# Performance work log

Measured on AMD Instinct MI355X. Metric: run time of the kernel, lower is better.

## Reference

```python
import jax, jax.numpy as jnp
import numpy as np

B, P, Q, N, D = 64, 12, 12, 1024, 64
DOW, TOD = 7, 288  # day-of-week / time-of-day one-hot depths (GMAN STEmbedding)


def setup_inputs() -> dict:
    key = jax.random.key(0)
    ks = iter(jax.random.split(key, 40))
    def g(shape, scale=0.05):
        return jax.random.normal(next(ks), shape, jnp.float32) * scale
    inp = {
        "X": jax.random.normal(next(ks), (B, P, N), jnp.float32),
        "ZC": jax.random.normal(next(ks), (B, P, 400), jnp.float32),
        "ZF": jax.random.normal(next(ks), (B, P, 1600), jnp.float32),
        "SE": g((N, D)),
        # STEmbedding FCs
        "W_se1": g((D, D)), "b_se1": jnp.zeros((D,), jnp.float32),
        "W_se2": g((D, D)), "b_se2": jnp.zeros((D,), jnp.float32),
        "W_te1": g((DOW + TOD, D)), "b_te1": jnp.zeros((D,), jnp.float32),
        "W_te2": g((D, D)), "b_te2": jnp.zeros((D,), jnp.float32),
        # FC_X_in
        "W_in1": g((1, D)), "b_in1": jnp.zeros((D,), jnp.float32),
        "W_in2": g((D, D)), "b_in2": jnp.zeros((D,), jnp.float32),
        # DCGRU layer 1 (gconv over [x||state, support@(x||state)] -> 4D input)
        "Wg1": g((4 * D, 2 * D)), "bg1": jnp.ones((2 * D,), jnp.float32),
        "Wc1": g((4 * D, D)), "bc1": jnp.zeros((D,), jnp.float32),
        # DCGRU layer 2
        "Wg2": g((4 * D, 2 * D)), "bg2": jnp.ones((2 * D,), jnp.float32),
        "Wc2": g((4 * D, D)), "bc2": jnp.zeros((D,), jnp.float32),
        # FC_X_out
        "W_o1": g((D, D)), "b_o1": jnp.zeros((D,), jnp.float32),
        "W_o2": g((D, Q)), "b_o2": jnp.zeros((Q,), jnp.float32),
        "TE": jax.random.randint(next(ks), (B, P + Q, 2), 0, 7, jnp.int32),
    }
    return inp


def _dcgru_scan(x_seq, support, Wg, bg, Wc, bc):
    """x_seq: [B,P,N,D] -> (sequence [B,P,N,D], last state [B,N,D])."""
    def gconv(x, s, W, b):
        z = jnp.concatenate([x, s], -1)                      # [B,N,2D]
        z1 = jnp.einsum('nm,bmd->bnd', support, z)           # diffusion step K=1
        return jnp.concatenate([z, z1], -1) @ W + b

    def step(state, x_t):
        ru = jax.nn.sigmoid(gconv(x_t, state, Wg, bg))       # [B,N,2D]
        r, u = jnp.split(ru, 2, axis=-1)
        c = jnp.tanh(gconv(x_t, r * state, Wc, bc))
        new = u * state + (1.0 - u) * c
        return new, new

    state0 = jnp.zeros(x_seq.shape[:1] + x_seq.shape[2:], x_seq.dtype)
    last, seq = jax.lax.scan(step, state0, jnp.swapaxes(x_seq, 0, 1))
    return jnp.swapaxes(seq, 0, 1), last


def reference(X, ZC, ZF, SE, W_se1, b_se1, W_se2, b_se2, W_te1, b_te1,
              W_te2, b_te2, W_in1, b_in1, W_in2, b_in2,
              Wg1, bg1, Wc1, bc1, Wg2, bg2, Wc2, bc2,
              W_o1, b_o1, W_o2, b_o2, TE):
    # adjacency is identity in this module; random_walk(I).T == I
    adj = jnp.eye(N, dtype=jnp.float32)
    support = (adj / jnp.sum(adj, axis=1, keepdims=True)).T

    # STEmbedding: spatial + temporal embedding
    se = jax.nn.relu(SE @ W_se1 + b_se1) @ W_se2 + b_se2                 # [N,D]
    te_oh = jnp.concatenate([
        jax.nn.one_hot(TE[..., 0], DOW, dtype=jnp.float32),
        jax.nn.one_hot(TE[..., 1], TOD, dtype=jnp.float32)], -1)        # [B,P+Q,295]
    te = jax.nn.relu(te_oh @ W_te1 + b_te1) @ W_te2 + b_te2              # [B,P+Q,D]
    STEX = (se[None, None] + te[:, :, None, :])[:, :P]                   # [B,P,N,D]

    # FC_X_in on expanded X, add STE
    Xe = X[..., None]                                                    # [B,P,N,1]
    Xe = jax.nn.relu(Xe @ W_in1 + b_in1) @ W_in2 + b_in2                 # [B,P,N,D]
    Xe = Xe + STEX

    seq1, _ = _dcgru_scan(Xe, support, Wg1, bg1, Wc1, bc1)               # [B,P,N,D]
    _, h = _dcgru_scan(seq1, support, Wg2, bg2, Wc2, bc2)                # [B,N,D]

    Y = jax.nn.relu(h @ W_o1 + b_o1) @ W_o2 + b_o2                       # [B,N,Q]
    return jnp.transpose(Y, (0, 2, 1))                                   # [B,Q,N]
```

## Files before the change

kernel.cpp:

```cpp
#include <hip/hip_runtime.h>


#define NB 1024

typedef float f32x4 __attribute__((ext_vector_type(4)));
typedef __bf16 bf16x8 __attribute__((ext_vector_type(8)));
typedef int i32x4 __attribute__((ext_vector_type(4)));
typedef unsigned int u32;
typedef unsigned short u16;

#define MFMA(a, b, c) __builtin_amdgcn_mfma_f32_16x16x32_bf16(a, b, c, 0, 0, 0)

__device__ __forceinline__ float fexp(float x) {
    return __builtin_amdgcn_exp2f(x * 1.44269504088896341f);
}
__device__ __forceinline__ float fsigmoid(float x) {
    return __builtin_amdgcn_rcpf(1.0f + fexp(-x));
}
__device__ __forceinline__ float ftanh(float x) {
    return 1.0f - 2.0f * __builtin_amdgcn_rcpf(1.0f + fexp(2.0f * x));
}

__device__ __forceinline__ u32 packf(float v) {
    u32 u = __builtin_bit_cast(u32, v);
    u32 hb = u & 0xFFFF0000u;
    float lo = v - __builtin_bit_cast(float, hb);
    return hb | (__builtin_bit_cast(u32, lo) >> 16);
}
__device__ __forceinline__ float unpackf(u32 u) {
    return __builtin_bit_cast(float, u & 0xFFFF0000u)
         + __builtin_bit_cast(float, u << 16);
}

__device__ __forceinline__ bf16x8 ldfrag(const u16* p) {
    i32x4 t = *(const i32x4*)p;
    return __builtin_bit_cast(bf16x8, t);
}
__device__ __forceinline__ bf16x8 ldfragL(const u32* p) {
    i32x4 t = *(const i32x4*)p;
    return __builtin_bit_cast(bf16x8, t);
}
__device__ __forceinline__ void split8(f32x4 a0, f32x4 a1, bf16x8& hi, bf16x8& lo) {
    #pragma unroll
    for (int i = 0; i < 4; i++) {
        __bf16 h0 = (__bf16)a0[i]; hi[i] = h0;     lo[i] = (__bf16)(a0[i] - (float)h0);
        __bf16 h1 = (__bf16)a1[i]; hi[4 + i] = h1; lo[4 + i] = (__bf16)(a1[i] - (float)h1);
    }
}

#define SWZ(t) ((((t) & 3) << 3) ^ ((t) & 4) ^ (((t) & 8) << 1))
#define SW(t, k) ((t) * 64 + ((k) ^ SWZ(t)))

__device__ __forceinline__ void lda_packed(const u32* __restrict__ src, int m, int kk,
                                           bf16x8& hi, bf16x8& lo) {
    const int sk = kk ^ SWZ(m);
    i32x4 d0 = *(const i32x4*)(src + m * 64 + sk);
    i32x4 d1 = *(const i32x4*)(src + m * 64 + (sk ^ 4));
    i32x4 h, L;
    h[0] = (int)__builtin_amdgcn_perm((u32)d0[1], (u32)d0[0], 0x07060302u);
    h[1] = (int)__builtin_amdgcn_perm((u32)d0[3], (u32)d0[2], 0x07060302u);
    h[2] = (int)__builtin_amdgcn_perm((u32)d1[1], (u32)d1[0], 0x07060302u);
    h[3] = (int)__builtin_amdgcn_perm((u32)d1[3], (u32)d1[2], 0x07060302u);
    L[0] = (int)__builtin_amdgcn_perm((u32)d0[1], (u32)d0[0], 0x05040100u);
    L[1] = (int)__builtin_amdgcn_perm((u32)d0[3], (u32)d0[2], 0x05040100u);
    L[2] = (int)__builtin_amdgcn_perm((u32)d1[1], (u32)d1[0], 0x05040100u);
    L[3] = (int)__builtin_amdgcn_perm((u32)d1[3], (u32)d1[2], 0x05040100u);
    hi = __builtin_bit_cast(bf16x8, h);
    lo = __builtin_bit_cast(bf16x8, L);
}


__device__ __forceinline__ void wsplit(float v, u16* dhi, u16* dlo) {
    __bf16 h = (__bf16)v;
    __bf16 l = (__bf16)(v - (float)h);
    *dhi = __builtin_bit_cast(u16, h);
    *dlo = __builtin_bit_cast(u16, l);
}

__global__ void prep_gates(const float* __restrict__ Wg1, const float* __restrict__ Wg2,
                           u16* __restrict__ fr) {
    int i = blockIdx.x * 256 + threadIdx.x;
    if (i >= 4096) return;
    int layer = i >> 11, r = i & 2047;
    int w = r >> 9; r &= 511; int nt = r >> 8; r &= 255; int ks = r >> 6; int lane = r & 63;
    const float* Wg = layer ? Wg2 : Wg1;
    int n = lane & 15, q = lane >> 4;
    int col = nt ? (64 + w * 16 + n) : (w * 16 + n);
    u16* dst = fr + layer * 32768 + (((w * 2 + nt) * 4 + ks) * 2) * 512 + lane * 8;
    #pragma unroll
    for (int j = 0; j < 8; j++) {
        int k = ks * 32 + q * 8 + j;
        float v = Wg[k * 128 + col] + Wg[(k + 128) * 128 + col];
        wsplit(v, dst + j, dst + 512 + j);
    }
}

__global__ void prep_cand(const float* __restrict__ Wc1, const float* __restrict__ Wc2,
                          u16* __restrict__ fr) {
    int i = blockIdx.x * 256 + threadIdx.x;
    if (i >= 2048) return;
    int layer = i >> 10, r = i & 1023;
    int w = r >> 8; r &= 255; int ks = r >> 6; int lane = r & 63;
    const float* Wc = layer ? Wc2 : Wc1;
    int n = lane & 15, q = lane >> 4;
    int col = w * 16 + n;
    u16* dst = fr + 65536 + layer * 16384 + ((w * 4 + ks) * 2) * 512 + lane * 8;
    #pragma unroll
    for (int j = 0; j < 8; j++) {
        int k = ks * 32 + q * 8 + j;
        float v = Wc[k * 64 + col] + Wc[(k + 128) * 64 + col];
        wsplit(v, dst + j, dst + 512 + j);
    }
}

__global__ void prep_small(const float* __restrict__ Win2, const float* __restrict__ Wo1,
                           u16* __restrict__ fr) {
    int i = blockIdx.x * 256 + threadIdx.x;
    if (i >= 1024) return;
    int kind = i >> 9, r = i & 511;
    int w = r >> 7; r &= 127; int ks = r >> 6; int lane = r & 63;
    const float* W = kind ? Wo1 : Win2;
    int n = lane & 15, q = lane >> 4;
    int col = w * 16 + n;
    u16* dst = fr + 98304 + kind * 8192 + ((w * 2 + ks) * 2) * 512 + lane * 8;
    #pragma unroll
    for (int j = 0; j < 8; j++) {
        int k = ks * 32 + q * 8 + j;
        float v = W[k * 64 + col];
        wsplit(v, dst + j, dst + 512 + j);
    }
}

__global__ void prep_se(const float* __restrict__ SE, const float* __restrict__ W1,
                        const float* __restrict__ b1, const float* __restrict__ W2,
                        const float* __restrict__ b2, const float* __restrict__ bin2,
                        float* __restrict__ seB) {
    __shared__ float h[64];
    int n = blockIdx.x, d = threadIdx.x;
    float acc = b1[d];
    for (int k = 0; k < 64; k++) acc = fmaf(SE[n * 64 + k], W1[k * 64 + d], acc);
    h[d] = fmaxf(acc, 0.0f);
    __syncthreads();
    float acc2 = b2[d];
    for (int k = 0; k < 64; k++) acc2 = fmaf(h[k], W2[k * 64 + d], acc2);
    int nb = n >> 6, tok = n & 63;
    int mt = tok >> 4, q = (tok >> 2) & 3, r = tok & 3;
    int w = d >> 4, n16 = d & 15;
    seB[(((nb * 4 + w) * 64) + q * 16 + n16) * 16 + mt * 4 + r] = acc2 + bin2[d];
}

__global__ void prep_te(const int* __restrict__ TE, const float* __restrict__ W1,
                        const float* __restrict__ b1, const float* __restrict__ W2,
                        const float* __restrict__ b2, float* __restrict__ teo) {
    __shared__ float h[64];
    int bp = blockIdx.x;
    int b = bp / 12, p = bp - b * 12;
    int d = threadIdx.x;
    int dow = TE[(b * 24 + p) * 2 + 0];
    int tod = TE[(b * 24 + p) * 2 + 1];
    float v = W1[dow * 64 + d] + W1[(7 + tod) * 64 + d] + b1[d];
    h[d] = fmaxf(v, 0.0f);
    __syncthreads();
    float acc = b2[d];
    for (int k = 0; k < 64; k++) acc = fmaf(h[k], W2[k * 64 + d], acc);
    teo[bp * 64 + d] = acc;
}

__device__ __forceinline__ void gru_full(
    const u32* __restrict__ XIN, u32* __restrict__ S, u32* __restrict__ RS,
    const u16* __restrict__ frG, const u16* __restrict__ frC,
    float bgr, float bgu, float bcc, int l, int col) {
    const int n16 = l & 15, q = l >> 4;
    f32x4 accR[4], accU[4], accC[4];
    #pragma unroll
    for (int mt = 0; mt < 4; mt++) {
        accR[mt] = (f32x4)0.0f; accU[mt] = (f32x4)0.0f; accC[mt] = (f32x4)0.0f;
    }
    #pragma unroll
    for (int ks = 0; ks < 2; ks++) {
        bf16x8 gRh = ldfrag(frG + (ks * 2 + 0) * 512 + l * 8);
        bf16x8 gRl = ldfrag(frG + (ks * 2 + 1) * 512 + l * 8);
        bf16x8 gUh = ldfrag(frG + (8 + ks * 2 + 0) * 512 + l * 8);
        bf16x8 gUl = ldfrag(frG + (8 + ks * 2 + 1) * 512 + l * 8);
        bf16x8 bhiC = ldfrag(frC + (ks * 2 + 0) * 512 + l * 8);
        bf16x8 bloC = ldfrag(frC + (ks * 2 + 1) * 512 + l * 8);
        const int kk = ks * 32 + q * 8;
        #pragma unroll
        for (int mt = 0; mt < 4; mt++) {
            bf16x8 ahi, alo;
            lda_packed(XIN, mt * 16 + n16, kk, ahi, alo);
            accR[mt] = MFMA(ahi, gRh, accR[mt]);
            accR[mt] = MFMA(alo, gRh, accR[mt]);
            accR[mt] = MFMA(ahi, gRl, accR[mt]);
            accU[mt] = MFMA(ahi, gUh, accU[mt]);
            accU[mt] = MFMA(alo, gUh, accU[mt]);
            accU[mt] = MFMA(ahi, gUl, accU[mt]);
            accC[mt] = MFMA(ahi, bhiC, accC[mt]);
            accC[mt] = MFMA(alo, bhiC, accC[mt]);
            accC[mt] = MFMA(ahi, bloC, accC[mt]);
        }
    }
    #pragma unroll
    for (int ks = 2; ks < 4; ks++) {
        bf16x8 gRh = ldfrag(frG + (ks * 2 + 0) * 512 + l * 8);
        bf16x8 gRl = ldfrag(frG + (ks * 2 + 1) * 512 + l * 8);
        bf16x8 gUh = ldfrag(frG + (8 + ks * 2 + 0) * 512 + l * 8);
        bf16x8 gUl = ldfrag(frG + (8 + ks * 2 + 1) * 512 + l * 8);
        const int kk = (ks - 2) * 32 + q * 8;
        #pragma unroll
        for (int mt = 0; mt < 4; mt++) {
            bf16x8 ahi, alo;
            lda_packed(S, mt * 16 + n16, kk, ahi, alo);
            accR[mt] = MFMA(ahi, gRh, accR[mt]);
            accR[mt] = MFMA(alo, gRh, accR[mt]);
            accR[mt] = MFMA(ahi, gRl, accR[mt]);
            accU[mt] = MFMA(ahi, gUh, accU[mt]);
            accU[mt] = MFMA(alo, gUh, accU[mt]);
            accU[mt] = MFMA(ahi, gUl, accU[mt]);
        }
    }
    #pragma unroll
    for (int mt = 0; mt < 4; mt++)
        #pragma unroll
        for (int r = 0; r < 4; r++) {
            int tok = mt * 16 + q * 4 + r;
            int a = SW(tok, col);
            RS[a] = packf(fsigmoid(accR[mt][r] + bgr) * unpackf(S[a]));
        }
    __syncthreads();
    #pragma unroll
    for (int ks = 2; ks < 4; ks++) {
        bf16x8 bhi = ldfrag(frC + (ks * 2 + 0) * 512 + l * 8);
        bf16x8 blo = ldfrag(frC + (ks * 2 + 1) * 512 + l * 8);
        const int kk = (ks - 2) * 32 + q * 8;
        #pragma unroll
        for (int mt = 0; mt < 4; mt++) {
            bf16x8 ahi, alo;
            lda_packed(RS, mt * 16 + n16, kk, ahi, alo);
            accC[mt] = MFMA(ahi, bhi, accC[mt]);
            accC[mt] = MFMA(alo, bhi, accC[mt]);
            accC[mt] = MFMA(ahi, blo, accC[mt]);
        }
    }
    #pragma unroll
    for (int mt = 0; mt < 4; mt++)
        #pragma unroll
        for (int r = 0; r < 4; r++) {
            int tok = mt * 16 + q * 4 + r;
            int a = SW(tok, col);
            float u = fsigmoid(accU[mt][r] + bgu);
            float cnd = ftanh(accC[mt][r] + bcc);
            float sold = unpackf(S[a]);
            S[a] = packf(u * sold + (1.0f - u) * cnd);
        }
    __syncthreads();
}

__global__ __launch_bounds__(256, 2) void gman_main(
    const float* __restrict__ X, const float* __restrict__ ws,
    const float* __restrict__ Win1, const float* __restrict__ bin1,
    const float* __restrict__ bg1, const float* __restrict__ bc1,
    const float* __restrict__ bg2, const float* __restrict__ bc2,
    const float* __restrict__ bo1, const float* __restrict__ Wo2,
    const float* __restrict__ bo2, float* __restrict__ out) {
    __shared__ u32 XE[4096], S1[4096], S2[4096], RS[4096];
    __shared__ u32 FRX[4096];

    const int tid = threadIdx.x;
    const int l = tid & 63;
    const int w = tid >> 6;
    const int uw = __builtin_amdgcn_readfirstlane(w);
    const int n16 = l & 15, q = l >> 4;
    const int col = uw * 16 + n16;
    const int b = blockIdx.x >> 4;
    const int nb = blockIdx.x & 15;
    const int n0 = nb << 6;

    const u16* frU = (const u16*)ws;
    const u16* frG1 = frU + uw * 8192;
    const u16* frG2 = frU + 32768 + uw * 8192;
    const u16* frC1 = frU + 65536 + uw * 4096;
    const u16* frC2 = frU + 81920 + uw * 4096;
    const u16* frH  = frU + 106496 + uw * 2048;
    const float* seQ = ws + 57344 + (((nb * 4 + uw) * 64) + l) * 16;
    const float* teo = ws + 122880;

    const u32* frXsrc = (const u32*)ws + 49152;
    #pragma unroll
    for (int i = 0; i < 16; i++) FRX[tid + i * 256] = frXsrc[tid + i * 256];
    const u32* frXL = FRX + uw * 1024;

    #pragma unroll
    for (int i = 0; i < 16; i++) { S1[tid + i * 256] = 0u; S2[tid + i * 256] = 0u; }

    f32x4 se_v[4];
    #pragma unroll
    for (int mt = 0; mt < 4; mt++) se_v[mt] = *(const f32x4*)(seQ + mt * 4);
    const float bg1r = bg1[col], bg1u = bg1[64 + col], bc1c = bc1[col];
    const float bg2r = bg2[col], bg2u = bg2[64 + col], bc2c = bc2[col];

    #pragma unroll 1
    for (int p = 0; p < 12; p++) {
        if (tid < 64) RS[tid] = __builtin_bit_cast(u32, X[(b * 12 + p) * NB + n0 + tid]);
        __syncthreads();
        f32x4 accX[4];
        #pragma unroll
        for (int mt = 0; mt < 4; mt++) accX[mt] = (f32x4)0.0f;
        #pragma unroll
        for (int ks = 0; ks < 2; ks++) {
            const int k0 = ks * 32 + q * 8;
            f32x4 w1a = *(const f32x4*)(Win1 + k0), w1b = *(const f32x4*)(Win1 + k0 + 4);
            f32x4 b1a = *(const f32x4*)(bin1 + k0), b1b = *(const f32x4*)(bin1 + k0 + 4);
            bf16x8 bhi = ldfragL(frXL + (ks * 2 + 0) * 256 + l * 4);
            bf16x8 blo = ldfragL(frXL + (ks * 2 + 1) * 256 + l * 4);
            #pragma unroll
            for (int mt = 0; mt < 4; mt++) {
                const float xm = __builtin_bit_cast(float, RS[mt * 16 + n16]);
                f32x4 h0, h1v;
                #pragma unroll
                for (int i = 0; i < 4; i++) {
                    h0[i]  = fmaxf(fmaf(xm, w1a[i], b1a[i]), 0.0f);
                    h1v[i] = fmaxf(fmaf(xm, w1b[i], b1b[i]), 0.0f);
                }
                bf16x8 ahi, alo; split8(h0, h1v, ahi, alo);
                accX[mt] = MFMA(ahi, bhi, accX[mt]);
                accX[mt] = MFMA(alo, bhi, accX[mt]);
                accX[mt] = MFMA(ahi, blo, accX[mt]);
            }
        }
        const float tev = teo[(b * 12 + p) * 64 + col];
        __syncthreads();
        #pragma unroll
        for (int mt = 0; mt < 4; mt++)
            #pragma unroll
            for (int r = 0; r < 4; r++) {
                int tok = mt * 16 + q * 4 + r;
                XE[SW(tok, col)] = packf(accX[mt][r] + se_v[mt][r] + tev);
            }
        __syncthreads();

        gru_full(XE, S1, RS, frG1, frC1, bg1r, bg1u, bc1c, l, col);
        gru_full(S1, S2, RS, frG2, frC2, bg2r, bg2u, bc2c, l, col);
    }

    f32x4 accH[4];
    #pragma unroll
    for (int mt = 0; mt < 4; mt++) accH[mt] = (f32x4)0.0f;
    #pragma unroll
    for (int ks = 0; ks < 2; ks++) {
        bf16x8 bhi = ldfrag(frH + (ks * 2 + 0) * 512 + l * 8);
        bf16x8 blo = ldfrag(frH + (ks * 2 + 1) * 512 + l * 8);
        const int kk = ks * 32 + q * 8;
        #pragma unroll
        for (int mt = 0; mt < 4; mt++) {
            bf16x8 ahi, alo;
            lda_packed(S2, mt * 16 + n16, kk, ahi, alo);
            accH[mt] = MFMA(ahi, bhi, accH[mt]);
            accH[mt] = MFMA(alo, bhi, accH[mt]);
            accH[mt] = MFMA(ahi, blo, accH[mt]);
        }
    }
    const float bo1c = bo1[col];
    #pragma unroll
    for (int mt = 0; mt < 4; mt++)
        #pragma unroll
        for (int r = 0; r < 4; r++) {
            int tok = mt * 16 + q * 4 + r;
            XE[SW(tok, col)] = packf(fmaxf(accH[mt][r] + bo1c, 0.0f));
        }
    __syncthreads();
    const int swzt = SWZ(l);
    float y0 = bo2[3 * uw + 0], y1 = bo2[3 * uw + 1], y2 = bo2[3 * uw + 2];
    #pragma unroll
    for (int c = 0; c < 16; c++) {
        i32x4 d = *(const i32x4*)(XE + l * 64 + c * 4);
        const int j0 = (c * 4) ^ swzt;
        #pragma unroll
        for (int e = 0; e < 4; e++) {
            float hj = unpackf((u32)d[e]);
            int j = j0 + e;
            y0 = fmaf(hj, Wo2[j * 12 + 3 * uw + 0], y0);
            y1 = fmaf(hj, Wo2[j * 12 + 3 * uw + 1], y1);
            y2 = fmaf(hj, Wo2[j * 12 + 3 * uw + 2], y2);
        }
    }
    out[(b * 12 + 3 * uw + 0) * NB + n0 + l] = y0;
    out[(b * 12 + 3 * uw + 1) * NB + n0 + l] = y1;
    out[(b * 12 + 3 * uw + 2) * NB + n0 + l] = y2;
}

extern "C" void kernel_launch(void* const* d_in, const int* in_sizes, int n_in,
                              void* d_out, int out_size, void* d_ws, size_t ws_size,
                              hipStream_t stream) {
    const float* X    = (const float*)d_in[0];
    const float* SE   = (const float*)d_in[3];
    const float* Wse1 = (const float*)d_in[4];
    const float* bse1 = (const float*)d_in[5];
    const float* Wse2 = (const float*)d_in[6];
    const float* bse2 = (const float*)d_in[7];
    const float* Wte1 = (const float*)d_in[8];
    const float* bte1 = (const float*)d_in[9];
    const float* Wte2 = (const float*)d_in[10];
    const float* bte2 = (const float*)d_in[11];
    const float* Win1 = (const float*)d_in[12];
    const float* bin1 = (const float*)d_in[13];
    const float* Win2 = (const float*)d_in[14];
    const float* bin2 = (const float*)d_in[15];
    const float* Wg1  = (const float*)d_in[16];
    const float* bg1  = (const float*)d_in[17];
    const float* Wc1  = (const float*)d_in[18];
    const float* bc1  = (const float*)d_in[19];
    const float* Wg2  = (const float*)d_in[20];
    const float* bg2  = (const float*)d_in[21];
    const float* Wc2  = (const float*)d_in[22];
    const float* bc2  = (const float*)d_in[23];
    const float* Wo1  = (const float*)d_in[24];
    const float* bo1  = (const float*)d_in[25];
    const float* Wo2  = (const float*)d_in[26];
    const float* bo2  = (const float*)d_in[27];
    const int*   TE   = (const int*)d_in[28];

    float* ws = (float*)d_ws;
    u16* fr = (u16*)ws;
    float* seB = ws + 57344;
    float* teo = ws + 122880;
    float* out = (float*)d_out;

    prep_gates<<<16, 256, 0, stream>>>(Wg1, Wg2, fr);
    prep_cand<<<8, 256, 0, stream>>>(Wc1, Wc2, fr);
    prep_small<<<4, 256, 0, stream>>>(Win2, Wo1, fr);
    prep_se<<<1024, 64, 0, stream>>>(SE, Wse1, bse1, Wse2, bse2, bin2, seB);
    prep_te<<<768, 64, 0, stream>>>(TE, Wte1, bte1, Wte2, bte2, teo);
    gman_main<<<1024, 256, 0, stream>>>(X, ws, Win1, bin1, bg1, bc1, bg2, bc2,
                                        bo1, Wo2, bo2, out);
}
```

Measured before the change: 554.8 us.

## Split each block's 64 tokens across two wave groups using 512 threads

Doubles the block to 512 threads (8 waves). Each group of four waves takes half of the 64 node tokens, which halves the per-wave MFMA M-tiles and accumulator registers in the GRU steps, the input projection and the output head. The goal is more waves per block to hide MFMA and LDS latency in the serial recurrence. In exchange, the same B-fragment weights are loaded by twice as many waves, and the 80KB of shared memory per block may limit how many blocks fit on each CU.

```diff
diff --git a/kernel.cpp b/kernel.cpp
--- a/kernel.cpp
+++ b/kernel.cpp
@@ -169,11 +169,11 @@
 __device__ __forceinline__ void gru_full(
     const u32* __restrict__ XIN, u32* __restrict__ S, u32* __restrict__ RS,
     const u16* __restrict__ frG, const u16* __restrict__ frC,
-    float bgr, float bgu, float bcc, int l, int col) {
+    float bgr, float bgu, float bcc, int l, int col, int mh) {
     const int n16 = l & 15, q = l >> 4;
-    f32x4 accR[4], accU[4], accC[4];
-    #pragma unroll
-    for (int mt = 0; mt < 4; mt++) {
+    f32x4 accR[2], accU[2], accC[2];
+    #pragma unroll
+    for (int mt = 0; mt < 2; mt++) {
         accR[mt] = (f32x4)0.0f; accU[mt] = (f32x4)0.0f; accC[mt] = (f32x4)0.0f;
     }
     #pragma unroll
@@ -186,9 +186,9 @@
         bf16x8 bloC = ldfrag(frC + (ks * 2 + 1) * 512 + l * 8);
         const int kk = ks * 32 + q * 8;
         #pragma unroll
-        for (int mt = 0; mt < 4; mt++) {
+        for (int mt = 0; mt < 2; mt++) {
             bf16x8 ahi, alo;
-            lda_packed(XIN, mt * 16 + n16, kk, ahi, alo);
+            lda_packed(XIN, mh * 32 + mt * 16 + n16, kk, ahi, alo);
             accR[mt] = MFMA(ahi, gRh, accR[mt]);
             accR[mt] = MFMA(alo, gRh, accR[mt]);
             accR[mt] = MFMA(ahi, gRl, accR[mt]);
@@ -208,9 +208,9 @@
         bf16x8 gUl = ldfrag(frG + (8 + ks * 2 + 1) * 512 + l * 8);
         const int kk = (ks - 2) * 32 + q * 8;
         #pragma unroll
-        for (int mt = 0; mt < 4; mt++) {
+        for (int mt = 0; mt < 2; mt++) {
             bf16x8 ahi, alo;
-            lda_packed(S, mt * 16 + n16, kk, ahi, alo);
+            lda_packed(S, mh * 32 + mt * 16 + n16, kk, ahi, alo);
             accR[mt] = MFMA(ahi, gRh, accR[mt]);
             accR[mt] = MFMA(alo, gRh, accR[mt]);
             accR[mt] = MFMA(ahi, gRl, accR[mt]);
@@ -220,10 +220,10 @@
         }
     }
     #pragma unroll
-    for (int mt = 0; mt < 4; mt++)
+    for (int mt = 0; mt < 2; mt++)
         #pragma unroll
         for (int r = 0; r < 4; r++) {
-            int tok = mt * 16 + q * 4 + r;
+            int tok = mh * 32 + mt * 16 + q * 4 + r;
             int a = SW(tok, col);
             RS[a] = packf(fsigmoid(accR[mt][r] + bgr) * unpackf(S[a]));
         }
@@ -234,19 +234,19 @@
         bf16x8 blo = ldfrag(frC + (ks * 2 + 1) * 512 + l * 8);
         const int kk = (ks - 2) * 32 + q * 8;
         #pragma unroll
-        for (int mt = 0; mt < 4; mt++) {
+        for (int mt = 0; mt < 2; mt++) {
             bf16x8 ahi, alo;
-            lda_packed(RS, mt * 16 + n16, kk, ahi, alo);
+            lda_packed(RS, mh * 32 + mt * 16 + n16, kk, ahi, alo);
             accC[mt] = MFMA(ahi, bhi, accC[mt]);
             accC[mt] = MFMA(alo, bhi, accC[mt]);
             accC[mt] = MFMA(ahi, blo, accC[mt]);
         }
     }
     #pragma unroll
-    for (int mt = 0; mt < 4; mt++)
+    for (int mt = 0; mt < 2; mt++)
         #pragma unroll
         for (int r = 0; r < 4; r++) {
-            int tok = mt * 16 + q * 4 + r;
+            int tok = mh * 32 + mt * 16 + q * 4 + r;
             int a = SW(tok, col);
             float u = fsigmoid(accU[mt][r] + bgu);
             float cnd = ftanh(accC[mt][r] + bcc);
@@ -256,7 +256,7 @@
     __syncthreads();
 }
 
-__global__ __launch_bounds__(256, 2) void gman_main(
+__global__ __launch_bounds__(512, 2) void gman_main(
     const float* __restrict__ X, const float* __restrict__ ws,
     const float* __restrict__ Win1, const float* __restrict__ bin1,
     const float* __restrict__ bg1, const float* __restrict__ bc1,
@@ -270,32 +270,34 @@
     const int l = tid & 63;
     const int w = tid >> 6;
     const int uw = __builtin_amdgcn_readfirstlane(w);
+    const int uq = uw & 3;
+    const int mh = uw >> 2;
     const int n16 = l & 15, q = l >> 4;
-    const int col = uw * 16 + n16;
+    const int col = uq * 16 + n16;
     const int b = blockIdx.x >> 4;
     const int nb = blockIdx.x & 15;
     const int n0 = nb << 6;
 
     const u16* frU = (const u16*)ws;
-    const u16* frG1 = frU + uw * 8192;
-    const u16* frG2 = frU + 32768 + uw * 8192;
-    const u16* frC1 = frU + 65536 + uw * 4096;
-    const u16* frC2 = frU + 81920 + uw * 4096;
-    const u16* frH  = frU + 106496 + uw * 2048;
-    const float* seQ = ws + 57344 + (((nb * 4 + uw) * 64) + l) * 16;
+    const u16* frG1 = frU + uq * 8192;
+    const u16* frG2 = frU + 32768 + uq * 8192;
+    const u16* frC1 = frU + 65536 + uq * 4096;
+    const u16* frC2 = frU + 81920 + uq * 4096;
+    const u16* frH  = frU + 106496 + uq * 2048;
+    const float* seQ = ws + 57344 + (((nb * 4 + uq) * 64) + l) * 16;
     const float* teo = ws + 122880;
 
     const u32* frXsrc = (const u32*)ws + 49152;
     #pragma unroll
-    for (int i = 0; i < 16; i++) FRX[tid + i * 256] = frXsrc[tid + i * 256];
-    const u32* frXL = FRX + uw * 1024;
-
-    #pragma unroll
-    for (int i = 0; i < 16; i++) { S1[tid + i * 256] = 0u; S2[tid + i * 256] = 0u; }
-
-    f32x4 se_v[4];
-    #pragma unroll
-    for (int mt = 0; mt < 4; mt++) se_v[mt] = *(const f32x4*)(seQ + mt * 4);
+    for (int i = 0; i < 8; i++) FRX[tid + i * 512] = frXsrc[tid + i * 512];
+    const u32* frXL = FRX + uq * 1024;
+
+    #pragma unroll
+    for (int i = 0; i < 8; i++) { S1[tid + i * 512] = 0u; S2[tid + i * 512] = 0u; }
+
+    f32x4 se_v[2];
+    #pragma unroll
+    for (int mt = 0; mt < 2; mt++) se_v[mt] = *(const f32x4*)(seQ + (mh * 2 + mt) * 4);
     const float bg1r = bg1[col], bg1u = bg1[64 + col], bc1c = bc1[col];
     const float bg2r = bg2[col], bg2u = bg2[64 + col], bc2c = bc2[col];
 
@@ -303,9 +305,9 @@
     for (int p = 0; p < 12; p++) {
         if (tid < 64) RS[tid] = __builtin_bit_cast(u32, X[(b * 12 + p) * NB + n0 + tid]);
         __syncthreads();
-        f32x4 accX[4];
-        #pragma unroll
-        for (int mt = 0; mt < 4; mt++) accX[mt] = (f32x4)0.0f;
+        f32x4 accX[2];
+        #pragma unroll
+        for (int mt = 0; mt < 2; mt++) accX[mt] = (f32x4)0.0f;
         #pragma unroll
         for (int ks = 0; ks < 2; ks++) {
             const int k0 = ks * 32 + q * 8;
@@ -314,8 +316,8 @@
             bf16x8 bhi = ldfragL(frXL + (ks * 2 + 0) * 256 + l * 4);
             bf16x8 blo = ldfragL(frXL + (ks * 2 + 1) * 256 + l * 4);
             #pragma unroll
-            for (int mt = 0; mt < 4; mt++) {
-                const float xm = __builtin_bit_cast(float, RS[mt * 16 + n16]);
+            for (int mt = 0; mt < 2; mt++) {
+                const float xm = __builtin_bit_cast(float, RS[mh * 32 + mt * 16 + n16]);
                 f32x4 h0, h1v;
                 #pragma unroll
                 for (int i = 0; i < 4; i++) {
@@ -331,30 +333,30 @@
         const float tev = teo[(b * 12 + p) * 64 + col];
         __syncthreads();
         #pragma unroll
-        for (int mt = 0; mt < 4; mt++)
+        for (int mt = 0; mt < 2; mt++)
             #pragma unroll
             for (int r = 0; r < 4; r++) {
-                int tok = mt * 16 + q * 4 + r;
+                int tok = mh * 32 + mt * 16 + q * 4 + r;
                 XE[SW(tok, col)] = packf(accX[mt][r] + se_v[mt][r] + tev);
             }
         __syncthreads();
 
-        gru_full(XE, S1, RS, frG1, frC1, bg1r, bg1u, bc1c, l, col);
-        gru_full(S1, S2, RS, frG2, frC2, bg2r, bg2u, bc2c, l, col);
-    }
-
-    f32x4 accH[4];
-    #pragma unroll
-    for (int mt = 0; mt < 4; mt++) accH[mt] = (f32x4)0.0f;
+        gru_full(XE, S1, RS, frG1, frC1, bg1r, bg1u, bc1c, l, col, mh);
+        gru_full(S1, S2, RS, frG2, frC2, bg2r, bg2u, bc2c, l, col, mh);
+    }
+
+    f32x4 accH[2];
+    #pragma unroll
+    for (int mt = 0; mt < 2; mt++) accH[mt] = (f32x4)0.0f;
     #pragma unroll
     for (int ks = 0; ks < 2; ks++) {
         bf16x8 bhi = ldfrag(frH + (ks * 2 + 0) * 512 + l * 8);
         bf16x8 blo = ldfrag(frH + (ks * 2 + 1) * 512 + l * 8);
         const int kk = ks * 32 + q * 8;
         #pragma unroll
-        for (int mt = 0; mt < 4; mt++) {
+        for (int mt = 0; mt < 2; mt++) {
             bf16x8 ahi, alo;
-            lda_packed(S2, mt * 16 + n16, kk, ahi, alo);
+            lda_packed(S2, mh * 32 + mt * 16 + n16, kk, ahi, alo);
             accH[mt] = MFMA(ahi, bhi, accH[mt]);
             accH[mt] = MFMA(alo, bhi, accH[mt]);
             accH[mt] = MFMA(ahi, blo, accH[mt]);
@@ -362,31 +364,33 @@
     }
     const float bo1c = bo1[col];
     #pragma unroll
-    for (int mt = 0; mt < 4; mt++)
+    for (int mt = 0; mt < 2; mt++)
         #pragma unroll
         for (int r = 0; r < 4; r++) {
-            int tok = mt * 16 + q * 4 + r;
+            int tok = mh * 32 + mt * 16 + q * 4 + r;
             XE[SW(tok, col)] = packf(fmaxf(accH[mt][r] + bo1c, 0.0f));
         }
     __syncthreads();
-    const int swzt = SWZ(l);
-    float y0 = bo2[3 * uw + 0], y1 = bo2[3 * uw + 1], y2 = bo2[3 * uw + 2];
-    #pragma unroll
-    for (int c = 0; c < 16; c++) {
-        i32x4 d = *(const i32x4*)(XE + l * 64 + c * 4);
-        const int j0 = (c * 4) ^ swzt;
-        #pragma unroll
-        for (int e = 0; e < 4; e++) {
-            float hj = unpackf((u32)d[e]);
-            int j = j0 + e;
-            y0 = fmaf(hj, Wo2[j * 12 + 3 * uw + 0], y0);
-            y1 = fmaf(hj, Wo2[j * 12 + 3 * uw + 1], y1);
-            y2 = fmaf(hj, Wo2[j * 12 + 3 * uw + 2], y2);
-        }
-    }
-    out[(b * 12 + 3 * uw + 0) * NB + n0 + l] = y0;
-    out[(b * 12 + 3 * uw + 1) * NB + n0 + l] = y1;
-    out[(b * 12 + 3 * uw + 2) * NB + n0 + l] = y2;
+    if (uw < 4) {
+        const int swzt = SWZ(l);
+        float y0 = bo2[3 * uw + 0], y1 = bo2[3 * uw + 1], y2 = bo2[3 * uw + 2];
+        #pragma unroll
+        for (int c = 0; c < 16; c++) {
+            i32x4 d = *(const i32x4*)(XE + l * 64 + c * 4);
+            const int j0 = (c * 4) ^ swzt;
+            #pragma unroll
+            for (int e = 0; e < 4; e++) {
+                float hj = unpackf((u32)d[e]);
+                int j = j0 + e;
+                y0 = fmaf(hj, Wo2[j * 12 + 3 * uw + 0], y0);
+                y1 = fmaf(hj, Wo2[j * 12 + 3 * uw + 1], y1);
+                y2 = fmaf(hj, Wo2[j * 12 + 3 * uw + 2], y2);
+            }
+        }
+        out[(b * 12 + 3 * uw + 0) * NB + n0 + l] = y0;
+        out[(b * 12 + 3 * uw + 1) * NB + n0 + l] = y1;
+        out[(b * 12 + 3 * uw + 2) * NB + n0 + l] = y2;
+    }
 }
 
 extern "C" void kernel_launch(void* const* d_in, const int* in_sizes, int n_in,
@@ -431,6 +435,6 @@
     prep_small<<<4, 256, 0, stream>>>(Win2, Wo1, fr);
     prep_se<<<1024, 64, 0, stream>>>(SE, Wse1, bse1, Wse2, bse2, bin2, seB);
     prep_te<<<768, 64, 0, stream>>>(TE, Wte1, bte1, Wte2, bte2, teo);
-    gman_main<<<1024, 256, 0, stream>>>(X, ws, Win1, bin1, bg1, bc1, bg2, bc2,
+    gman_main<<<1024, 512, 0, stream>>>(X, ws, Win1, bin1, bg1, bc1, bg2, bc2,
                                         bo1, Wo2, bo2, out);
 }
```

After: 718.6 us. 1.3x slower.
